# Kernel tuning notes

Measured on AMD Instinct MI355X. Metric: run time of the kernel, lower is better.

The kernel has to match this reference:

```python
import jax, jax.numpy as jnp
import numpy as np

B, T, C, H = 2, 2048, 2048, 16
HD = C // H      # 128 head dim
P = C // 8       # 256 octonion component width
NEG_INF = jnp.finfo(jnp.float32).min

# Cayley octonion multiplication table: e_i * e_j = OCT_SIGN[i,j] * e_{OCT_IDX[i,j]}
OCT_SIGN = np.array([
    [1, 1, 1, 1, 1, 1, 1, 1],
    [1,-1, 1,-1, 1,-1,-1, 1],
    [1,-1,-1, 1, 1, 1,-1,-1],
    [1, 1,-1,-1, 1,-1, 1,-1],
    [1,-1,-1,-1,-1, 1, 1, 1],
    [1, 1,-1, 1,-1,-1,-1, 1],
    [1, 1, 1,-1,-1, 1,-1,-1],
    [1,-1, 1, 1,-1,-1, 1,-1]], dtype=np.float32)
OCT_IDX = np.array([
    [0,1,2,3,4,5,6,7],
    [1,0,3,2,5,4,7,6],
    [2,3,0,1,6,7,4,5],
    [3,2,1,0,7,6,5,4],
    [4,5,6,7,0,1,2,3],
    [5,4,7,6,1,0,3,2],
    [6,7,4,5,2,3,0,1],
    [7,6,5,4,3,2,1,0]], dtype=np.int32)
_comb = np.zeros((8, 8, 8), np.float32)
for _i in range(8):
    for _j in range(8):
        _comb[OCT_IDX[_i, _j], _i, _j] = OCT_SIGN[_i, _j]
COMB = jnp.asarray(_comb)  # (k, i, j): out_k += sign * (W_i @ x_j)


def ternary(W):
    # BitNet-style ternary quantization with straight-through estimator
    s = jnp.mean(jnp.abs(W)) + 1e-8
    q = jnp.round(jnp.clip(W / s, -1.0, 1.0)) * s
    return W + jax.lax.stop_gradient(q - W)


def oct_linear(x, W):
    # x: (B,T,C), W: (8,P,P) -> (B,T,C)
    parts = jnp.stack(jnp.split(x, 8, axis=-1), axis=0)  # (8,B,T,P)
    Wq = ternary(W)
    prod = jnp.einsum('jbtp,ipq->ijbtq', parts, Wq)       # (8,8,B,T,P)
    out = jnp.einsum('kij,ijbtq->kbtq', COMB, prod)       # (8,B,T,P)
    return jnp.transpose(out, (1, 2, 0, 3)).reshape(x.shape[0], x.shape[1], C)


def rope(x, cos, sin):
    # x: (B,T,H,HD); cos/sin: (T, HD//2). Interleaved complex pairs as in view_as_complex.
    xr = x[..., 0::2]
    xi = x[..., 1::2]
    c = cos[None, :x.shape[1], None, :]
    s = sin[None, :x.shape[1], None, :]
    out = jnp.stack([xr * c - xi * s, xr * s + xi * c], axis=-1)
    return out.reshape(x.shape)


def setup_inputs() -> dict:
    key = jax.random.key(0)
    ks = jax.random.split(key, 5)
    x = jax.random.normal(ks[0], (B, T, C), dtype=jnp.float32)
    wq = jax.random.normal(ks[1], (8, P, P), dtype=jnp.float32) * 0.02
    wk = jax.random.normal(ks[2], (8, P, P), dtype=jnp.float32) * 0.02
    wv = jax.random.normal(ks[3], (8, P, P), dtype=jnp.float32) * 0.02
    wo = jax.random.normal(ks[4], (8, P, P), dtype=jnp.float32) * 0.02
    inv = 1.0 / (10000.0 ** (np.arange(0, HD, 2, dtype=np.float32) / HD))
    ang = np.outer(np.arange(T, dtype=np.float32), inv)
    freqs_cos = jnp.asarray(np.cos(ang), dtype=jnp.float32)
    freqs_sin = jnp.asarray(np.sin(ang), dtype=jnp.float32)
    return {"x": x, "wq": wq, "wk": wk, "wv": wv, "wo": wo,
            "freqs_cos": freqs_cos, "freqs_sin": freqs_sin}


def reference(x, wq, wk, wv, wo, freqs_cos, freqs_sin):
    b, t, _ = x.shape
    q = oct_linear(x, wq).reshape(b, t, H, HD)
    k = oct_linear(x, wk).reshape(b, t, H, HD)
    v = oct_linear(x, wv).reshape(b, t, H, HD)
    q = rope(q, freqs_cos, freqs_sin)
    k = rope(k, freqs_cos, freqs_sin)
    q = jnp.transpose(q, (0, 2, 1, 3))  # (B,H,T,HD)
    k = jnp.transpose(k, (0, 2, 1, 3))
    v = jnp.transpose(v, (0, 2, 1, 3))
    scores = jnp.einsum('bhtd,bhsd->bhts', q, k) / jnp.sqrt(jnp.float32(HD))
    mask = jnp.tril(jnp.ones((t, t), dtype=bool))
    scores = jnp.where(mask[None, None], scores, NEG_INF)
    attn = jax.nn.softmax(scores, axis=-1)
    y = jnp.einsum('bhts,bhsd->bhtd', attn, v)
    y = jnp.transpose(y, (0, 2, 1, 3)).reshape(b, t, C)
    return oct_linear(y, wo)
```

## Files before the change

### kernel.cpp

```cpp
#include <hip/hip_runtime.h>


typedef __attribute__((ext_vector_type(8))) short short8;
typedef __attribute__((ext_vector_type(4))) float f32x4;
typedef unsigned short u16;
typedef unsigned int u32;

__device__ __forceinline__ float bf2f(u16 u) {
    u32 x = ((u32)u) << 16;
    return __builtin_bit_cast(float, x);
}
__device__ __forceinline__ u16 f2bf(float f) {
    u32 x = __builtin_bit_cast(u32, f);
    x += 0x7fffu + ((x >> 16) & 1u);
    return (u16)(x >> 16);
}
__device__ __forceinline__ u16 f2bf_trunc(float f) {
    return (u16)(__builtin_bit_cast(u32, f) >> 16);
}
__device__ __forceinline__ u32 pack2(u16 a, u16 b) { return (u32)a | ((u32)b << 16); }

__device__ __forceinline__ void async16(const void* g, void* l) {
    __builtin_amdgcn_global_load_lds((const __attribute__((address_space(1))) u32*)g,
                                     (__attribute__((address_space(3))) u32*)l, 16, 0, 0);
}

__device__ const int d_OCT_IDX[8][8] = {
    {0,1,2,3,4,5,6,7},{1,0,3,2,5,4,7,6},{2,3,0,1,6,7,4,5},{3,2,1,0,7,6,5,4},
    {4,5,6,7,0,1,2,3},{5,4,7,6,1,0,3,2},{6,7,4,5,2,3,0,1},{7,6,5,4,3,2,1,0}};
__device__ const float d_OCT_SIGN[8][8] = {
    { 1, 1, 1, 1, 1, 1, 1, 1},{ 1,-1, 1,-1, 1,-1,-1, 1},{ 1,-1,-1, 1, 1, 1,-1,-1},
    { 1, 1,-1,-1, 1,-1, 1,-1},{ 1,-1,-1,-1,-1, 1, 1, 1},{ 1, 1,-1, 1,-1,-1,-1, 1},
    { 1, 1, 1,-1,-1, 1,-1,-1},{ 1,-1, 1, 1,-1,-1, 1,-1}};

__global__ __launch_bounds__(256) void reduce1_kernel(
    const float* __restrict__ w0, const float* __restrict__ w1,
    const float* __restrict__ w2, const float* __restrict__ w3,
    float* __restrict__ partials) {
    int bid = blockIdx.x, wsel = bid >> 6, part = bid & 63;
    const float* W = wsel == 0 ? w0 : wsel == 1 ? w1 : wsel == 2 ? w2 : w3;
    int base = part * 8192 + threadIdx.x;
    float acc = 0.f;
#pragma unroll
    for (int k = 0; k < 32; k++) acc += fabsf(W[base + k * 256]);
#pragma unroll
    for (int off = 1; off < 64; off <<= 1) acc += __shfl_xor(acc, off, 64);
    __shared__ float r4[4];
    if ((threadIdx.x & 63) == 0) r4[threadIdx.x >> 6] = acc;
    __syncthreads();
    if (threadIdx.x == 0) partials[bid] = r4[0] + r4[1] + r4[2] + r4[3];
}
__global__ __launch_bounds__(256) void reduce2_kernel(const float* __restrict__ partials,
                                                      float* __restrict__ s_vals) {
    int w = threadIdx.x >> 6, lane = threadIdx.x & 63;
    float v = partials[w * 64 + lane];
#pragma unroll
    for (int off = 1; off < 64; off <<= 1) v += __shfl_xor(v, off, 64);
    if (lane == 0) s_vals[w] = v / 524288.0f + 1e-8f;
}

__global__ __launch_bounds__(256) void cast_bf16_kernel(const float* __restrict__ X, u16* __restrict__ Xb) {
    int gid = blockIdx.x * 256 + threadIdx.x;
    const float4* X4 = (const float4*)X;
    float4 a = X4[gid * 2], b = X4[gid * 2 + 1];
    uint4 o;
    o.x = pack2(f2bf(a.x), f2bf(a.y));
    o.y = pack2(f2bf(a.z), f2bf(a.w));
    o.z = pack2(f2bf(b.x), f2bf(b.y));
    o.w = pack2(f2bf(b.z), f2bf(b.w));
    *(uint4*)&Xb[gid * 8] = o;
}

__global__ __launch_bounds__(256) void build_weff_kernel(
    const float* __restrict__ W, const float* __restrict__ sptr, u16* __restrict__ WT) {
    __shared__ float Tt[64 * 68];
    int tid = threadIdx.x;
    int combo = blockIdx.x >> 4, sub = blockIdx.x & 15;
    int j = combo >> 3, kblk = combo & 7;
    int i = 0;
#pragma unroll
    for (int ii = 0; ii < 8; ii++)
        if (d_OCT_IDX[ii][j] == kblk) i = ii;
    float sign = d_OCT_SIGN[i][j];
    int p0 = (sub >> 2) * 64, q0 = (sub & 3) * 64;
    float inv_s = 1.0f / (*sptr);
#pragma unroll
    for (int pass = 0; pass < 4; pass++) {
        int p = p0 + pass * 16 + (tid >> 4);
        int q = q0 + (tid & 15) * 4;
        float4 wv = *(const float4*)&W[i * 65536 + p * 256 + q];
        float* Tp = &Tt[(pass * 16 + (tid >> 4)) * 68 + (tid & 15) * 4];
        Tp[0] = sign * rintf(fminf(1.f, fmaxf(-1.f, wv.x * inv_s)));
        Tp[1] = sign * rintf(fminf(1.f, fmaxf(-1.f, wv.y * inv_s)));
        Tp[2] = sign * rintf(fminf(1.f, fmaxf(-1.f, wv.z * inv_s)));
        Tp[3] = sign * rintf(fminf(1.f, fmaxf(-1.f, wv.w * inv_s)));
    }
    __syncthreads();
#pragma unroll
    for (int pass = 0; pass < 2; pass++) {
        int qq = pass * 32 + (tid >> 3);
        int pl = (tid & 7) * 8;
        u16 r[8];
#pragma unroll
        for (int l = 0; l < 8; l++) r[l] = f2bf_trunc(Tt[(pl + l) * 68 + qq]);
        uint4 o;
        o.x = pack2(r[0], r[1]); o.y = pack2(r[2], r[3]);
        o.z = pack2(r[4], r[5]); o.w = pack2(r[6], r[7]);
        *(uint4*)&WT[(size_t)(kblk * 256 + q0 + qq) * 2048 + j * 256 + p0 + pl] = o;
    }
}

template <int MODE>
__global__ __launch_bounds__(256) void gemm_kernel(
    const u16* __restrict__ A, const u16* __restrict__ Bt,
    const float* __restrict__ sptr, void* __restrict__ Cout) {
    __shared__ __align__(16) u16 As[128 * 32];
    __shared__ __align__(16) u16 Bs[128 * 32];
    const int K = 2048;
    int tid = threadIdx.x, lane = tid & 63, wid = tid >> 6;
    int quad = lane >> 4, l16 = lane & 15;
    int wm = (wid >> 1) * 64, wn = (wid & 1) * 64;
    int m0 = blockIdx.y * 128, n0 = blockIdx.x * 128;
    f32x4 acc[4][4];
#pragma unroll
    for (int a = 0; a < 4; a++)
#pragma unroll
        for (int b = 0; b < 4; b++) acc[a][b] = (f32x4){0.f, 0.f, 0.f, 0.f};
    int srow = lane >> 2;
    int sblk = (lane & 3) ^ (srow & 3);
    const u16* Ag = A + (size_t)(m0 + wid * 32 + srow) * K + sblk * 8;
    const u16* Bg = Bt + (size_t)(n0 + wid * 32 + srow) * K + sblk * 8;
    u16* Al = &As[(wid * 32) * 32];
    u16* Bl = &Bs[(wid * 32) * 32];
    int rblk = (quad ^ (l16 & 3)) * 8;
    for (int k0 = 0; k0 < K; k0 += 32) {
        __syncthreads();
        async16(Ag + k0, Al);
        async16(Ag + k0 + (size_t)16 * K, Al + 16 * 32);
        async16(Bg + k0, Bl);
        async16(Bg + k0 + (size_t)16 * K, Bl + 16 * 32);
        __syncthreads();
        short8 af[4], bfv[4];
#pragma unroll
        for (int mt = 0; mt < 4; mt++) af[mt] = *(const short8*)&As[(wm + mt * 16 + l16) * 32 + rblk];
#pragma unroll
        for (int nt = 0; nt < 4; nt++) bfv[nt] = *(const short8*)&Bs[(wn + nt * 16 + l16) * 32 + rblk];
#pragma unroll
        for (int mt = 0; mt < 4; mt++)
#pragma unroll
            for (int nt = 0; nt < 4; nt++)
                acc[mt][nt] = __builtin_amdgcn_mfma_f32_16x16x32_bf16(af[mt], bfv[nt], acc[mt][nt], 0, 0, 0);
    }
    float s = *sptr;
#pragma unroll
    for (int mt = 0; mt < 4; mt++)
#pragma unroll
        for (int nt = 0; nt < 4; nt++) {
            int mg = m0 + wm + mt * 16 + quad * 4;
            int ng = n0 + wn + nt * 16 + l16;
            if (MODE == 0) {
#pragma unroll
                for (int r = 0; r < 4; r++)
                    ((u16*)Cout)[(size_t)(mg + r) * 2048 + ng] = f2bf(acc[mt][nt][r] * s);
            } else if (MODE == 1) {
#pragma unroll
                for (int r = 0; r < 4; r++)
                    ((float*)Cout)[(size_t)(mg + r) * 2048 + ng] = acc[mt][nt][r] * s;
            } else {
                ushort4 o4;
                o4.x = f2bf(acc[mt][nt][0] * s);
                o4.y = f2bf(acc[mt][nt][1] * s);
                o4.z = f2bf(acc[mt][nt][2] * s);
                o4.w = f2bf(acc[mt][nt][3] * s);
                *(ushort4*)&((u16*)Cout)[((size_t)((mg >> 11) * 16 + (ng >> 7)) * 128 + (ng & 127)) * 2048 + (mg & 2047)] = o4;
            }
        }
}

__global__ __launch_bounds__(256) void rope_kernel(
    u16* __restrict__ Xb, const float* __restrict__ fc, const float* __restrict__ fs, float scale) {
    int gid = blockIdx.x * 256 + threadIdx.x;
    int c2 = gid & 1023;
    int t = (gid >> 10) & 2047;
    int m = c2 & 63;
    u32 u = ((u32*)Xb)[gid];
    float xr = bf2f((u16)(u & 0xffff));
    float xi = bf2f((u16)(u >> 16));
    float c = fc[t * 64 + m] * scale, s = fs[t * 64 + m] * scale;
    ((u32*)Xb)[gid] = pack2(f2bf(xr * c - xi * s), f2bf(xr * s + xi * c));
}

__global__ __launch_bounds__(512, 2) void flash_kernel(
    const u16* __restrict__ Q, const u16* __restrict__ Kg,
    const u16* __restrict__ VTg, u16* __restrict__ Y) {
    __shared__ __align__(16) u16 Ks[2][64 * 128];
    __shared__ __align__(16) u16 Vs[2][128 * 64];
    __shared__ __align__(16) u16 Ps[8 * 16 * 64];
    const int NIT = 34;
    int tid = threadIdx.x, lane = tid & 63, wid = tid >> 6;
    int quad = lane >> 4, l16 = lane & 15;
    int bh = blockIdx.x, b = bh >> 4, h = bh & 15;
    int qt = blockIdx.y;
    int nitA = 2 * qt + 2;
    const u16* Qb = Q + (size_t)b * 2048 * 2048 + h * 128;
    const u16* Kb = Kg + (size_t)b * 2048 * 2048 + h * 128;
    const u16* Vb = VTg + (size_t)bh * 128 * 2048;
    int q0 = qt * 128, nit = nitA;
    int ksr = lane >> 4, ksb = lane & 15;
    int vsr = lane >> 3, vsb = lane & 7;
#pragma unroll
    for (int cc = 0; cc < 2; cc++) {
        int ch = wid * 2 + cc;
        int kr = ch * 4 + ksr;
        async16(&Kb[(size_t)kr * 2048 + (ksb ^ (kr & 15)) * 8], &Ks[0][ch * 512]);
        int vd = ch * 8 + vsr;
        async16(&Vb[(size_t)vd * 2048 + (vsb ^ (vd & 7)) * 8], &Vs[0][ch * 512]);
    }
    short8 qf[4];
#pragma unroll
    for (int kt = 0; kt < 4; kt++)
        qf[kt] = *(const short8*)&Qb[(size_t)(q0 + wid * 16 + l16) * 2048 + kt * 32 + quad * 8];
    f32x4 o[8];
#pragma unroll
    for (int nt = 0; nt < 8; nt++) o[nt] = (f32x4){0.f, 0.f, 0.f, 0.f};
    float m_[4] = {-1e30f, -1e30f, -1e30f, -1e30f};
    float l_[4] = {0.f, 0.f, 0.f, 0.f};
    int il = 0;
    for (int g = 0; g < NIT; g++) {
        int c = g & 1;
        __syncthreads();
        if (g + 1 < NIT) {
            int gn = g + 1;
            int s0n = (gn < nitA ? gn : gn - nitA) * 64;
#pragma unroll
            for (int cc = 0; cc < 2; cc++) {
                int ch = wid * 2 + cc;
                int kr = ch * 4 + ksr;
                async16(&Kb[(size_t)(s0n + kr) * 2048 + (ksb ^ (kr & 15)) * 8], &Ks[1 - c][ch * 512]);
                int vd = ch * 8 + vsr;
                async16(&Vb[(size_t)vd * 2048 + s0n + (vsb ^ (vd & 7)) * 8], &Vs[1 - c][ch * 512]);
            }
        }
        int s0 = il * 64;
        f32x4 sc[4];
#pragma unroll
        for (int ct = 0; ct < 4; ct++) {
            f32x4 a = (f32x4){0.f, 0.f, 0.f, 0.f};
#pragma unroll
            for (int kt = 0; kt < 4; kt++) {
                short8 bfv = *(const short8*)&Ks[c][(ct * 16 + l16) * 128 + ((kt * 4 + quad) ^ l16) * 8];
                a = __builtin_amdgcn_mfma_f32_16x16x32_bf16(qf[kt], bfv, a, 0, 0, 0);
            }
            sc[ct] = a;
        }
        if (il >= nit - 2) {
#pragma unroll
            for (int ct = 0; ct < 4; ct++) {
                int colg = s0 + ct * 16 + l16;
#pragma unroll
                for (int r = 0; r < 4; r++) {
                    int rowg = q0 + wid * 16 + quad * 4 + r;
                    if (colg > rowg) sc[ct][r] = -1e30f;
                }
            }
        }
        float alpha[4];
#pragma unroll
        for (int r = 0; r < 4; r++) {
            float mx = fmaxf(fmaxf(sc[0][r], sc[1][r]), fmaxf(sc[2][r], sc[3][r]));
#pragma unroll
            for (int off = 1; off < 16; off <<= 1) mx = fmaxf(mx, __shfl_xor(mx, off, 64));
            float mn = fmaxf(m_[r], mx);
            float al = exp2f(m_[r] - mn);
            float rs = 0.f;
#pragma unroll
            for (int ct = 0; ct < 4; ct++) {
                float p = exp2f(sc[ct][r] - mn);
                sc[ct][r] = p;
                rs += p;
            }
#pragma unroll
            for (int off = 1; off < 16; off <<= 1) rs += __shfl_xor(rs, off, 64);
            m_[r] = mn;
            l_[r] = l_[r] * al + rs;
            alpha[r] = al;
        }
        u16* Pw = &Ps[wid * 1024];
#pragma unroll
        for (int ct = 0; ct < 4; ct++)
#pragma unroll
            for (int r = 0; r < 4; r++) {
                int lr = quad * 4 + r;
                int key = ct * 16 + l16;
                Pw[lr * 64 + ((key >> 3) ^ (lr & 7)) * 8 + (key & 7)] = f2bf_trunc(sc[ct][r]);
            }
#pragma unroll
        for (int nt = 0; nt < 8; nt++)
#pragma unroll
            for (int r = 0; r < 4; r++) o[nt][r] *= alpha[r];
#pragma unroll
        for (int kt2 = 0; kt2 < 2; kt2++) {
            short8 pa = *(const short8*)&Pw[l16 * 64 + ((kt2 * 4 + quad) ^ (l16 & 7)) * 8];
#pragma unroll
            for (int nt = 0; nt < 8; nt++) {
                short8 vb = *(const short8*)&Vs[c][(nt * 16 + l16) * 64 + ((kt2 * 4 + quad) ^ (l16 & 7)) * 8];
                o[nt] = __builtin_amdgcn_mfma_f32_16x16x32_bf16(pa, vb, o[nt], 0, 0, 0);
            }
        }
        il++;
        if (il == nit && g + 1 < NIT) {
            float iv[4];
#pragma unroll
            for (int r = 0; r < 4; r++) iv[r] = 1.f / l_[r];
#pragma unroll
            for (int nt = 0; nt < 8; nt++)
#pragma unroll
                for (int r = 0; r < 4; r++) {
                    int t_ = q0 + wid * 16 + quad * 4 + r;
                    Y[((size_t)(b * 2048 + t_)) * 2048 + h * 128 + nt * 16 + l16] = f2bf(o[nt][r] * iv[r]);
                }
            q0 = (15 - qt) * 128;
            nit = NIT - nitA;
            il = 0;
#pragma unroll
            for (int kt = 0; kt < 4; kt++)
                qf[kt] = *(const short8*)&Qb[(size_t)(q0 + wid * 16 + l16) * 2048 + kt * 32 + quad * 8];
#pragma unroll
            for (int nt = 0; nt < 8; nt++) o[nt] = (f32x4){0.f, 0.f, 0.f, 0.f};
#pragma unroll
            for (int r = 0; r < 4; r++) { m_[r] = -1e30f; l_[r] = 0.f; }
        }
    }
    float iv[4];
#pragma unroll
    for (int r = 0; r < 4; r++) iv[r] = 1.f / l_[r];
#pragma unroll
    for (int nt = 0; nt < 8; nt++)
#pragma unroll
        for (int r = 0; r < 4; r++) {
            int t_ = q0 + wid * 16 + quad * 4 + r;
            Y[((size_t)(b * 2048 + t_)) * 2048 + h * 128 + nt * 16 + l16] = f2bf(o[nt][r] * iv[r]);
        }
}

extern "C" void kernel_launch(void* const* d_in, const int* in_sizes, int n_in,
                              void* d_out, int out_size, void* d_ws, size_t ws_size,
                              hipStream_t stream) {
    const float* x  = (const float*)d_in[0];
    const float* wq = (const float*)d_in[1];
    const float* wk = (const float*)d_in[2];
    const float* wv = (const float*)d_in[3];
    const float* wo = (const float*)d_in[4];
    const float* fc = (const float*)d_in[5];
    const float* fs = (const float*)d_in[6];
    float* out = (float*)d_out;

    char* ws = (char*)d_ws;
    float* s_vals   = (float*)ws;
    float* partials = (float*)(ws + 1024);
    u16* WT  = (u16*)(ws + 8192);
    u16* xb  = (u16*)(ws + 8192 + 8388608);
    u16* Qb  = xb + 8388608;
    u16* Kb  = Qb + 8388608;
    u16* VTb = Kb + 8388608;

    const float QSCALE = 0.08838834764831845f * 1.4426950408889634f;

    reduce1_kernel<<<256, 256, 0, stream>>>(wq, wk, wv, wo, partials);
    reduce2_kernel<<<1, 256, 0, stream>>>(partials, s_vals);
    cast_bf16_kernel<<<4096, 256, 0, stream>>>(x, xb);

    build_weff_kernel<<<1024, 256, 0, stream>>>(wq, s_vals + 0, WT);
    gemm_kernel<0><<<dim3(16, 32), 256, 0, stream>>>(xb, WT, s_vals + 0, Qb);
    rope_kernel<<<16384, 256, 0, stream>>>(Qb, fc, fs, QSCALE);

    build_weff_kernel<<<1024, 256, 0, stream>>>(wk, s_vals + 1, WT);
    gemm_kernel<0><<<dim3(16, 32), 256, 0, stream>>>(xb, WT, s_vals + 1, Kb);
    rope_kernel<<<16384, 256, 0, stream>>>(Kb, fc, fs, 1.0f);

    build_weff_kernel<<<1024, 256, 0, stream>>>(wv, s_vals + 2, WT);
    gemm_kernel<2><<<dim3(16, 32), 256, 0, stream>>>(xb, WT, s_vals + 2, VTb);

    flash_kernel<<<dim3(32, 8), 512, 0, stream>>>(Qb, Kb, VTb, Qb );

    build_weff_kernel<<<1024, 256, 0, stream>>>(wo, s_vals + 3, WT);
    gemm_kernel<1><<<dim3(16, 32), 256, 0, stream>>>(Qb, WT, s_vals + 3, (void*)out);
}
```

Baseline: 415.2 us.

## Double-buffer GEMM with 64-wide K tiles, vectorize rope, add MFMA priority hints

The GEMM kernel now uses double-buffered LDS tiles of K=64, issuing async loads for the next tile while computing the current one. This halves the barriers per K step and overlaps global loads with MFMA work, at the cost of four times the LDS per block. The rope kernel processes four complex pairs per thread with vector loads and launches a quarter as many blocks. The flash kernel raises wave priority around its MFMA sections to improve interleaving between waves.

```diff
diff --git a/kernel.cpp b/kernel.cpp
--- a/kernel.cpp
+++ b/kernel.cpp
@@ -114,9 +114,10 @@
 __global__ __launch_bounds__(256) void gemm_kernel(
     const u16* __restrict__ A, const u16* __restrict__ Bt,
     const float* __restrict__ sptr, void* __restrict__ Cout) {
-    __shared__ __align__(16) u16 As[128 * 32];
-    __shared__ __align__(16) u16 Bs[128 * 32];
+    __shared__ __align__(16) u16 As[2][128 * 64];
+    __shared__ __align__(16) u16 Bs[2][128 * 64];
     const int K = 2048;
+    const int NIT = K / 64;
     int tid = threadIdx.x, lane = tid & 63, wid = tid >> 6;
     int quad = lane >> 4, l16 = lane & 15;
     int wm = (wid >> 1) * 64, wn = (wid & 1) * 64;
@@ -126,30 +127,40 @@
     for (int a = 0; a < 4; a++)
 #pragma unroll
         for (int b = 0; b < 4; b++) acc[a][b] = (f32x4){0.f, 0.f, 0.f, 0.f};
-    int srow = lane >> 2;
-    int sblk = (lane & 3) ^ (srow & 3);
-    const u16* Ag = A + (size_t)(m0 + wid * 32 + srow) * K + sblk * 8;
-    const u16* Bg = Bt + (size_t)(n0 + wid * 32 + srow) * K + sblk * 8;
-    u16* Al = &As[(wid * 32) * 32];
-    u16* Bl = &Bs[(wid * 32) * 32];
-    int rblk = (quad ^ (l16 & 3)) * 8;
-    for (int k0 = 0; k0 < K; k0 += 32) {
+    int sr = lane >> 3, sb = lane & 7;
+    const u16* Ag = A + (size_t)(m0 + wid * 32 + sr) * K + ((sb ^ sr) * 8);
+    const u16* Bg = Bt + (size_t)(n0 + wid * 32 + sr) * K + ((sb ^ sr) * 8);
+#pragma unroll
+    for (int cc = 0; cc < 4; cc++) {
+        async16(Ag + (size_t)cc * 8 * K, &As[0][(wid * 32 + cc * 8) * 64]);
+        async16(Bg + (size_t)cc * 8 * K, &Bs[0][(wid * 32 + cc * 8) * 64]);
+    }
+    for (int g = 0; g < NIT; g++) {
+        int c = g & 1;
         __syncthreads();
-        async16(Ag + k0, Al);
-        async16(Ag + k0 + (size_t)16 * K, Al + 16 * 32);
-        async16(Bg + k0, Bl);
-        async16(Bg + k0 + (size_t)16 * K, Bl + 16 * 32);
-        __syncthreads();
-        short8 af[4], bfv[4];
-#pragma unroll
-        for (int mt = 0; mt < 4; mt++) af[mt] = *(const short8*)&As[(wm + mt * 16 + l16) * 32 + rblk];
-#pragma unroll
-        for (int nt = 0; nt < 4; nt++) bfv[nt] = *(const short8*)&Bs[(wn + nt * 16 + l16) * 32 + rblk];
-#pragma unroll
-        for (int mt = 0; mt < 4; mt++)
+        if (g + 1 < NIT) {
+            int k1 = (g + 1) * 64;
+#pragma unroll
+            for (int cc = 0; cc < 4; cc++) {
+                async16(Ag + k1 + (size_t)cc * 8 * K, &As[1 - c][(wid * 32 + cc * 8) * 64]);
+                async16(Bg + k1 + (size_t)cc * 8 * K, &Bs[1 - c][(wid * 32 + cc * 8) * 64]);
+            }
+        }
+#pragma unroll
+        for (int kc = 0; kc < 2; kc++) {
+            short8 af[4], bfv[4];
+#pragma unroll
+            for (int mt = 0; mt < 4; mt++)
+                af[mt] = *(const short8*)&As[c][(wm + mt * 16 + l16) * 64 + (((kc << 2) | quad) ^ (l16 & 7)) * 8];
 #pragma unroll
             for (int nt = 0; nt < 4; nt++)
-                acc[mt][nt] = __builtin_amdgcn_mfma_f32_16x16x32_bf16(af[mt], bfv[nt], acc[mt][nt], 0, 0, 0);
+                bfv[nt] = *(const short8*)&Bs[c][(wn + nt * 16 + l16) * 64 + (((kc << 2) | quad) ^ (l16 & 7)) * 8];
+#pragma unroll
+            for (int mt = 0; mt < 4; mt++)
+#pragma unroll
+                for (int nt = 0; nt < 4; nt++)
+                    acc[mt][nt] = __builtin_amdgcn_mfma_f32_16x16x32_bf16(af[mt], bfv[nt], acc[mt][nt], 0, 0, 0);
+        }
     }
     float s = *sptr;
 #pragma unroll
@@ -177,17 +188,26 @@
         }
 }
 
+__device__ __forceinline__ u32 rope_rot(u32 u, float c, float s) {
+    float xr = bf2f((u16)(u & 0xffff));
+    float xi = bf2f((u16)(u >> 16));
+    return pack2(f2bf(xr * c - xi * s), f2bf(xr * s + xi * c));
+}
 __global__ __launch_bounds__(256) void rope_kernel(
     u16* __restrict__ Xb, const float* __restrict__ fc, const float* __restrict__ fs, float scale) {
     int gid = blockIdx.x * 256 + threadIdx.x;
-    int c2 = gid & 1023;
-    int t = (gid >> 10) & 2047;
-    int m = c2 & 63;
-    u32 u = ((u32*)Xb)[gid];
-    float xr = bf2f((u16)(u & 0xffff));
-    float xi = bf2f((u16)(u >> 16));
-    float c = fc[t * 64 + m] * scale, s = fs[t * 64 + m] * scale;
-    ((u32*)Xb)[gid] = pack2(f2bf(xr * c - xi * s), f2bf(xr * s + xi * c));
+    int e0 = gid * 4;
+    int t = (e0 >> 10) & 2047;
+    int m = e0 & 63;
+    uint4 u = ((const uint4*)Xb)[gid];
+    float4 c4 = *(const float4*)&fc[t * 64 + m];
+    float4 s4 = *(const float4*)&fs[t * 64 + m];
+    uint4 o;
+    o.x = rope_rot(u.x, c4.x * scale, s4.x * scale);
+    o.y = rope_rot(u.y, c4.y * scale, s4.y * scale);
+    o.z = rope_rot(u.z, c4.z * scale, s4.z * scale);
+    o.w = rope_rot(u.w, c4.w * scale, s4.w * scale);
+    ((uint4*)Xb)[gid] = o;
 }
 
 __global__ __launch_bounds__(512, 2) void flash_kernel(
@@ -243,6 +263,7 @@
         }
         int s0 = il * 64;
         f32x4 sc[4];
+        __builtin_amdgcn_s_setprio(1);
 #pragma unroll
         for (int ct = 0; ct < 4; ct++) {
             f32x4 a = (f32x4){0.f, 0.f, 0.f, 0.f};
@@ -253,6 +274,7 @@
             }
             sc[ct] = a;
         }
+        __builtin_amdgcn_s_setprio(0);
         if (il >= nit - 2) {
 #pragma unroll
             for (int ct = 0; ct < 4; ct++) {
@@ -298,6 +320,7 @@
         for (int nt = 0; nt < 8; nt++)
 #pragma unroll
             for (int r = 0; r < 4; r++) o[nt][r] *= alpha[r];
+        __builtin_amdgcn_s_setprio(1);
 #pragma unroll
         for (int kt2 = 0; kt2 < 2; kt2++) {
             short8 pa = *(const short8*)&Pw[l16 * 64 + ((kt2 * 4 + quad) ^ (l16 & 7)) * 8];
@@ -307,6 +330,7 @@
                 o[nt] = __builtin_amdgcn_mfma_f32_16x16x32_bf16(pa, vb, o[nt], 0, 0, 0);
             }
         }
+        __builtin_amdgcn_s_setprio(0);
         il++;
         if (il == nit && g + 1 < NIT) {
             float iv[4];
@@ -372,11 +396,11 @@
 
     build_weff_kernel<<<1024, 256, 0, stream>>>(wq, s_vals + 0, WT);
     gemm_kernel<0><<<dim3(16, 32), 256, 0, stream>>>(xb, WT, s_vals + 0, Qb);
-    rope_kernel<<<16384, 256, 0, stream>>>(Qb, fc, fs, QSCALE);
+    rope_kernel<<<4096, 256, 0, stream>>>(Qb, fc, fs, QSCALE);
 
     build_weff_kernel<<<1024, 256, 0, stream>>>(wk, s_vals + 1, WT);
     gemm_kernel<0><<<dim3(16, 32), 256, 0, stream>>>(xb, WT, s_vals + 1, Kb);
-    rope_kernel<<<16384, 256, 0, stream>>>(Kb, fc, fs, 1.0f);
+    rope_kernel<<<4096, 256, 0, stream>>>(Kb, fc, fs, 1.0f);
 
     build_weff_kernel<<<1024, 256, 0, stream>>>(wv, s_vals + 2, WT);
     gemm_kernel<2><<<dim3(16, 32), 256, 0, stream>>>(xb, WT, s_vals + 2, VTb);
```

After: 399.4 us. 3.8% less time.
